# Kernel tuning notes

Measured on AMD Instinct MI355X. Metric: run time of the kernel, lower is better.

Reference implementation:

```python
import jax, jax.numpy as jnp
import numpy as np

B, J, D, H, W, AE, GH, NA, EH, L = 64, 20000, 32, 64, 4, 16, 24, 5000, 128, 32


def _ln(x, g=None, b=None, eps=1e-5):
    mu = x.mean(-1, keepdims=True)
    var = jnp.mean((x - mu) ** 2, axis=-1, keepdims=True)
    y = (x - mu) * jax.lax.rsqrt(var + eps)
    if g is not None:
        y = y * g + b
    return y


def setup_inputs():
    key = jax.random.key(0)
    ks = jax.random.split(key, 12)
    def rn(k, shape, s):
        return (jax.random.normal(k, shape) * s).astype(jnp.float32)
    return {
        "x": jax.random.normal(ks[0], (B, J), jnp.float32),
        "mask": jax.random.randint(ks[1], (B, J), 0, 2, jnp.int32),
        "atse_idx": jax.random.randint(ks[2], (J,), 0, NA, jnp.int32),
        "feature_embedding": jax.random.normal(ks[3], (J, D), jnp.float32),
        "atse_embedding": jax.random.normal(ks[4], (NA, AE), jnp.float32),
        "h_W1": rn(ks[5], (1 + D, H), 0.15), "h_b1": jnp.zeros((H,), jnp.float32),
        "h_ln1_g": jnp.ones((H,), jnp.float32), "h_ln1_b": jnp.zeros((H,), jnp.float32),
        "h_W2": rn(ks[6], (H, D), 0.12), "h_b2": jnp.zeros((D,), jnp.float32),
        "h_ln2_g": jnp.ones((D,), jnp.float32), "h_ln2_b": jnp.zeros((D,), jnp.float32),
        "g_W1": rn(ks[7], (D + AE, GH), 0.14), "g_b1": jnp.zeros((GH,), jnp.float32),
        "g_W2": rn(ks[8], (GH, W), 0.2), "g_b2": jnp.zeros((W,), jnp.float32),
        "c_W": rn(ks[9], (W * D, D), 0.09), "c_b": jnp.zeros((D,), jnp.float32),
        "c_ln_g": jnp.ones((D,), jnp.float32), "c_ln_b": jnp.zeros((D,), jnp.float32),
        "e_W1": rn(ks[10], (D, EH), 0.18), "e_b1": jnp.zeros((EH,), jnp.float32),
        "e_W2": rn(ks[11], (EH, 2 * L), 0.09), "e_b2": jnp.zeros((2 * L,), jnp.float32),
    }


def _forward(x, mask, atse_idx, feature_embedding, atse_embedding,
             h_W1, h_b1, h_ln1_g, h_ln1_b, h_W2, h_b2, h_ln2_g, h_ln2_b,
             g_W1, g_b1, g_W2, g_b2, c_W, c_b, c_ln_g, c_ln_b,
             e_W1, e_b1, e_W2, e_b2):
    TEMP = 1.0  # temperature_fixed=True -> scale = temperature_value
    Bv, Jv = x.shape
    Dv = feature_embedding.shape[1]
    # h-layer on all (b, j) pairs; LayerNorm/ReLU are per-row so this equals the
    # per-sample gather version on observed rows (unobserved rows get zero weight below).
    h_in = jnp.concatenate(
        [x[..., None], jnp.broadcast_to(feature_embedding[None], (Bv, Jv, Dv))], axis=-1)
    h = jax.nn.relu(_ln(h_in @ h_W1 + h_b1, h_ln1_g, h_ln1_b))
    h_out = jax.nn.relu(_ln(h @ h_W2 + h_b2, h_ln2_g, h_ln2_b))  # [B, J, D]
    # gate: [h_out | E_atse(j)] -> W head logits
    ae = atse_embedding[atse_idx]  # [J, AE]
    gate_in = jnp.concatenate(
        [h_out, jnp.broadcast_to(ae[None], (Bv, Jv, ae.shape[1]))], axis=-1)
    raw = jax.nn.relu(gate_in @ g_W1 + g_b1) @ g_W2 + g_b2  # [B, J, W]
    logits = jnp.clip(raw * TEMP, -10.0, 10.0)
    obs = mask.astype(bool)
    masked = jnp.where(obs[..., None], logits, -1e9)
    weights = jax.nn.softmax(masked, axis=1)  # softmax over observed junctions per head
    head_sums = jnp.einsum('bjw,bjd->bwd', weights, h_out)  # [B, W, D]
    Wn, Dn = head_sums.shape[1], head_sums.shape[2]
    combined = jax.nn.relu(_ln(head_sums.reshape(Bv, Wn * Dn) @ c_W + c_b, c_ln_g, c_ln_b))
    combined = jnp.where(obs.any(axis=1)[:, None], combined, 0.0)  # empty-mask rows -> zeros
    # encoder_mlp: scvi FCLayers, 2 layers, LayerNorm (no affine) + ReLU each
    e1 = jax.nn.relu(_ln(combined @ e_W1 + e_b1))
    mu_logvar = jax.nn.relu(_ln(e1 @ e_W2 + e_b2))
    mu, logvar = jnp.split(mu_logvar, 2, axis=-1)
    return mu, logvar


def reference(x, mask, atse_idx, feature_embedding, atse_embedding,
              h_W1, h_b1, h_ln1_g, h_ln1_b, h_W2, h_b2, h_ln2_g, h_ln2_b,
              g_W1, g_b1, g_W2, g_b2, c_W, c_b, c_ln_g, c_ln_b,
              e_W1, e_b1, e_W2, e_b2):
    return _forward(x, mask, atse_idx, feature_embedding, atse_embedding,
                    h_W1, h_b1, h_ln1_g, h_ln1_b, h_W2, h_b2, h_ln2_g, h_ln2_b,
                    g_W1, g_b1, g_W2, g_b2, c_W, c_b, c_ln_g, c_ln_b,
                    e_W1, e_b1, e_W2, e_b2)
```

## Files before the change

kernel.cpp:

```cpp
#include <hip/hip_runtime.h>
#include <hip/hip_bf16.h>
#include <math.h>

#define Bv 64
#define Jv 20000
#define NJT 625
#define NBT 8

typedef __attribute__((ext_vector_type(8))) short short8;
typedef __attribute__((ext_vector_type(4))) float f32x4;

union U8 { short8 s; unsigned int u[4]; };

__device__ __forceinline__ unsigned short f2bf(float f) {
  unsigned int u = __float_as_uint(f);
  u += 0x7FFFu + ((u >> 16) & 1u);
  return (unsigned short)(u >> 16);
}
__device__ __forceinline__ unsigned int pkbf(float a, float b) {
  __hip_bfloat162 h = __float22bfloat162_rn(make_float2(a, b));
  union { __hip_bfloat162 h; unsigned int u; } c;
  c.h = h;
  return c.u;
}
__device__ __forceinline__ float bflo(unsigned int u) { return __uint_as_float(u << 16); }
__device__ __forceinline__ float bfhi(unsigned int u) { return __uint_as_float(u & 0xFFFF0000u); }

__global__ __launch_bounds__(256) void pe_fused(
    const float* __restrict__ x, const int* __restrict__ mask,
    const int* __restrict__ atse_idx, const float* __restrict__ fe,
    const float* __restrict__ ae,
    const float* __restrict__ hW1, const float* __restrict__ hb1,
    const float* __restrict__ hl1g, const float* __restrict__ hl1b,
    const float* __restrict__ hW2, const float* __restrict__ hb2,
    const float* __restrict__ hl2g, const float* __restrict__ hl2b,
    const float* __restrict__ gW1, const float* __restrict__ gb1,
    const float* __restrict__ gW2, const float* __restrict__ gb2,
    float* __restrict__ acc_g, float* __restrict__ se_g) {
  __shared__ __align__(16) float s_pg[32 * 68];
  __shared__ __align__(16) float s_ex[32 * 4];
  __shared__ __align__(16) float s_gb[32 * 28 + 16];
  __shared__ __align__(16) float s_pair[256 * 4];
  __shared__ __align__(16) float s_w0[64], s_w0g[64], s_l1g[64], s_l1b[64];
  __shared__ __align__(16) float s_b2[32], s_l2g[32], s_l2b[32];
  __shared__ __align__(16) float s_gb1[24], s_gW2[96];
  __shared__ float s_gb2[4], s_scal[2];
  __shared__ int s_mk[256];
  __shared__ __align__(16) unsigned short s_gW1bf[32 * 24];
  __shared__ __align__(16) unsigned short s_ovl[256 * 34];

  int tid = threadIdx.x;
  int btile = blockIdx.x;
  int jtile = blockIdx.y;
  int J0 = jtile * 32;
  int lane = tid & 63, wv = tid >> 6;
  int li = lane & 15, quad = lane >> 4;

  float* ovlf = (float*)s_ovl;
  float* s_aeo = ovlf + 2048;
  float* s_gW1bo = ovlf + 2688;
  unsigned short* s_h = s_ovl;

  for (int i = tid; i < 2048; i += 256) ovlf[i] = hW2[i];
  for (int i = tid; i < 768; i += 256) s_gW1bf[i] = f2bf(gW1[i]);
  for (int i = tid; i < 384; i += 256) s_gW1bo[i] = gW1[768 + i];
  if (tid < 96) s_gW2[tid] = gW2[tid];
  if (tid < 64) { s_w0[tid] = hW1[tid]; s_l1g[tid] = hl1g[tid]; s_l1b[tid] = hl1b[tid]; }
  if (tid < 32) { s_b2[tid] = hb2[tid]; s_l2g[tid] = hl2g[tid]; s_l2b[tid] = hl2b[tid]; }
  if (tid < 24) s_gb1[tid] = gb1[tid];
  if (tid < 4) s_gb2[tid] = gb2[tid];
  if (tid < 128) s_gb[(tid >> 2) * 28 + 24 + (tid & 3)] = 0.f;
  if (tid >= 128 && tid < 144) s_gb[32 * 28 + (tid - 128)] = 0.f;
  if (tid < 32) {
    int ai = atse_idx[J0 + tid];
    const float4* av = (const float4*)(ae + (size_t)ai * 16);
#pragma unroll
    for (int q = 0; q < 4; ++q) *(float4*)(s_aeo + tid * 20 + q * 4) = av[q];
  }
  __syncthreads();

  {
    U8 bH;
#pragma unroll
    for (int p = 0; p < 4; ++p) {
      float lo = hW1[(1 + quad * 8 + 2 * p) * 64 + wv * 16 + li];
      float hi = hW1[(1 + quad * 8 + 2 * p + 1) * 64 + wv * 16 + li];
      bH.u[p] = pkbf(lo, hi);
    }
    float hb = hb1[wv * 16 + li];
    f32x4 cP;
#pragma unroll
    for (int mt = 0; mt < 2; ++mt) {
      cP[0] = hb; cP[1] = hb; cP[2] = hb; cP[3] = hb;
      const float* fp = fe + (size_t)(J0 + mt * 16 + li) * 32 + quad * 8;
      float4 f0 = *(const float4*)fp;
      float4 f1 = *(const float4*)(fp + 4);
      U8 aF;
      aF.u[0] = pkbf(f0.x, f0.y); aF.u[1] = pkbf(f0.z, f0.w);
      aF.u[2] = pkbf(f1.x, f1.y); aF.u[3] = pkbf(f1.z, f1.w);
      cP = __builtin_amdgcn_mfma_f32_16x16x32_bf16(aF.s, bH.s, cP, 0, 0, 0);
#pragma unroll
      for (int r = 0; r < 4; ++r)
        s_pg[(mt * 16 + quad * 4 + r) * 68 + wv * 16 + li] = cP[r];
    }
  }
  {
    int jp = tid >> 3, ks = tid & 7;
    int c0 = ks * 3;
    float g3[3] = {s_gb1[c0], s_gb1[c0 + 1], s_gb1[c0 + 2]};
#pragma unroll 4
    for (int a = 0; a < 16; ++a) {
      float Av = s_aeo[jp * 20 + a];
      const float* gr = s_gW1bo + a * 24 + c0;
      g3[0] = fmaf(Av, gr[0], g3[0]);
      g3[1] = fmaf(Av, gr[1], g3[1]);
      g3[2] = fmaf(Av, gr[2], g3[2]);
    }
    s_gb[jp * 28 + c0] = g3[0];
    s_gb[jp * 28 + c0 + 1] = g3[1];
    s_gb[jp * 28 + c0 + 2] = g3[2];
  }
  __syncthreads();

  if (tid < 32) {
    float sp = 0.f, qp = 0.f, dwp = 0.f;
#pragma unroll 8
    for (int k = 0; k < 64; ++k) {
      float p = s_pg[tid * 68 + k];
      float w = s_w0[k];
      sp += p;
      qp = fmaf(p, p, qp);
      dwp = fmaf(p, w, dwp);
    }
    ((float4*)s_ex)[tid] = make_float4(sp, qp, dwp, 0.f);
  } else if (tid == 32) {
    float sw = 0.f, qw = 0.f;
    for (int k = 0; k < 64; ++k) {
      float w = s_w0[k];
      sw += w;
      qw = fmaf(w, w, qw);
    }
    s_scal[0] = sw;
    s_scal[1] = qw;
  } else if (tid >= 64 && tid < 128) {
    s_w0g[tid - 64] = s_w0[tid - 64] * s_l1g[tid - 64];
  }
  __syncthreads();

  {
    int jp = tid >> 3, ks = tid & 7;
    float* pp = s_pg + jp * 68 + ks * 8;
    float4 a0 = *(float4*)pp, a1 = *(float4*)(pp + 4);
    float4 g0 = *(float4*)(s_l1g + ks * 8), g1 = *(float4*)(s_l1g + ks * 8 + 4);
    a0.x *= g0.x; a0.y *= g0.y; a0.z *= g0.z; a0.w *= g0.w;
    a1.x *= g1.x; a1.y *= g1.y; a1.z *= g1.z; a1.w *= g1.w;
    *(float4*)pp = a0;
    *(float4*)(pp + 4) = a1;
  }
  short8 bW2[2][2];
#pragma unroll
  for (int kt = 0; kt < 2; ++kt)
#pragma unroll
    for (int nt = 0; nt < 2; ++nt) {
      U8 t;
#pragma unroll
      for (int p = 0; p < 4; ++p) {
        float lo = ovlf[(kt * 32 + quad * 8 + 2 * p) * 32 + nt * 16 + li];
        float hi = ovlf[(kt * 32 + quad * 8 + 2 * p + 1) * 32 + nt * 16 + li];
        t.u[p] = pkbf(lo, hi);
      }
      bW2[kt][nt] = t.s;
    }
  {
    int j = tid >> 3, b = tid & 7;
    size_t off = (size_t)(btile * 8 + b) * Jv + J0 + j;
    float xv = x[off];
    s_mk[tid] = mask[off];
    float4 ex = ((const float4*)s_ex)[j];
    float mu1 = fmaf(xv, s_scal[0], ex.x) * 0.015625f;
    float Et2 = fmaf(xv * xv, s_scal[1], fmaf(2.0f * xv, ex.z, ex.y)) * 0.015625f;
    float rs1 = rsqrtf(fmaxf(Et2 - mu1 * mu1, 0.f) + 1e-5f);
    *(float4*)(s_pair + tid * 4) = make_float4(xv * rs1, rs1, -mu1 * rs1, 0.f);
  }
  __syncthreads();

  {
    f32x4 cd[4][2];
    float b2a = s_b2[li], b2b = s_b2[16 + li];
#pragma unroll
    for (int t = 0; t < 4; ++t) {
      cd[t][0][0] = b2a; cd[t][0][1] = b2a; cd[t][0][2] = b2a; cd[t][0][3] = b2a;
      cd[t][1][0] = b2b; cd[t][1][1] = b2b; cd[t][1][2] = b2b; cd[t][1][3] = b2b;
    }
#pragma unroll
    for (int kt = 0; kt < 2; ++kt) {
      int base = kt * 32 + quad * 8;
      float4 wg0 = *(const float4*)(s_w0g + base);
      float4 wg1 = *(const float4*)(s_w0g + base + 4);
      float4 gg0 = *(const float4*)(s_l1g + base);
      float4 gg1 = *(const float4*)(s_l1g + base + 4);
      float4 bb0 = *(const float4*)(s_l1b + base);
      float4 bb1 = *(const float4*)(s_l1b + base + 4);
      float wg[8] = {wg0.x, wg0.y, wg0.z, wg0.w, wg1.x, wg1.y, wg1.z, wg1.w};
      float gg[8] = {gg0.x, gg0.y, gg0.z, gg0.w, gg1.x, gg1.y, gg1.z, gg1.w};
      float bb[8] = {bb0.x, bb0.y, bb0.z, bb0.w, bb1.x, bb1.y, bb1.z, bb1.w};
#pragma unroll
      for (int t = 0; t < 4; ++t) {
        int mrow = wv * 64 + t * 16 + li;
        float4 pr = *(const float4*)(s_pair + mrow * 4);
        const float* pgp = s_pg + (mrow >> 3) * 68 + base;
        float4 p0 = *(const float4*)pgp;
        float4 p1 = *(const float4*)(pgp + 4);
        float pv[8] = {p0.x, p0.y, p0.z, p0.w, p1.x, p1.y, p1.z, p1.w};
        float av[8];
#pragma unroll
        for (int i = 0; i < 8; ++i)
          av[i] = fmaxf(fmaf(pr.x, wg[i], fmaf(pr.y, pv[i], fmaf(pr.z, gg[i], bb[i]))), 0.f);
        U8 a8;
        a8.u[0] = pkbf(av[0], av[1]); a8.u[1] = pkbf(av[2], av[3]);
        a8.u[2] = pkbf(av[4], av[5]); a8.u[3] = pkbf(av[6], av[7]);
        cd[t][0] = __builtin_amdgcn_mfma_f32_16x16x32_bf16(a8.s, bW2[kt][0], cd[t][0], 0, 0, 0);
        cd[t][1] = __builtin_amdgcn_mfma_f32_16x16x32_bf16(a8.s, bW2[kt][1], cd[t][1], 0, 0, 0);
      }
    }
    float g0 = s_l2g[li], be0 = s_l2b[li];
    float g1v = s_l2g[16 + li], be1 = s_l2b[16 + li];
#pragma unroll
    for (int t = 0; t < 4; ++t) {
      float sum[4], sq[4];
#pragma unroll
      for (int r = 0; r < 4; ++r) {
        float a = cd[t][0][r], b = cd[t][1][r];
        sum[r] = a + b;
        sq[r] = fmaf(a, a, b * b);
      }
#pragma unroll
      for (int off = 1; off < 16; off <<= 1) {
#pragma unroll
        for (int r = 0; r < 4; ++r) {
          sum[r] += __shfl_xor(sum[r], off);
          sq[r] += __shfl_xor(sq[r], off);
        }
      }
#pragma unroll
      for (int r = 0; r < 4; ++r) {
        float mu = sum[r] * 0.03125f;
        float var = sq[r] * 0.03125f - mu * mu;
        float rs2 = rsqrtf(fmaxf(var, 0.f) + 1e-5f);
        int m = wv * 64 + t * 16 + quad * 4 + r;
        float h0 = fmaxf(fmaf((cd[t][0][r] - mu) * rs2, g0, be0), 0.f);
        float h1 = fmaxf(fmaf((cd[t][1][r] - mu) * rs2, g1v, be1), 0.f);
        s_h[m * 34 + li] = f2bf(h0);
        s_h[m * 34 + 16 + li] = f2bf(h1);
      }
    }
  }

  {
    short8 aG0, aG1;
#pragma unroll
    for (int i = 0; i < 8; ++i) {
      int k = quad * 8 + i;
      aG0[i] = (short)s_gW1bf[k * 24 + li];
      aG1[i] = (li < 8) ? (short)s_gW1bf[k * 24 + 16 + li] : (short)0;
    }
    float4 gw4[2][4];
#pragma unroll
    for (int mt = 0; mt < 2; ++mt)
#pragma unroll
      for (int r = 0; r < 4; ++r) {
        int c = mt * 16 + quad * 4 + r;
        gw4[mt][r] = (c < 24) ? ((const float4*)s_gW2)[c]
                              : make_float4(0.f, 0.f, 0.f, 0.f);
      }
#pragma unroll
    for (int nt = 0; nt < 4; ++nt) {
      int m = wv * 64 + nt * 16 + li;
      U8 bu;
      const unsigned short* hp = s_h + m * 34 + quad * 8;
      bu.u[0] = *(const unsigned int*)(hp + 0);
      bu.u[1] = *(const unsigned int*)(hp + 2);
      bu.u[2] = *(const unsigned int*)(hp + 4);
      bu.u[3] = *(const unsigned int*)(hp + 6);
      int j = m >> 3;
      f32x4 c0, c1;
#pragma unroll
      for (int r = 0; r < 4; ++r) {
        c0[r] = s_gb[j * 28 + quad * 4 + r];
        c1[r] = s_gb[j * 28 + 16 + quad * 4 + r];
      }
      c0 = __builtin_amdgcn_mfma_f32_16x16x32_bf16(aG0, bu.s, c0, 0, 0, 0);
      c1 = __builtin_amdgcn_mfma_f32_16x16x32_bf16(aG1, bu.s, c1, 0, 0, 0);
      float r0 = s_gb2[0], r1 = s_gb2[1], r2 = s_gb2[2], r3 = s_gb2[3];
#pragma unroll
      for (int r = 0; r < 4; ++r) {
        float v0 = fmaxf(c0[r], 0.f);
        float v1 = fmaxf(c1[r], 0.f);
        float4 ga = gw4[0][r], gb = gw4[1][r];
        r0 = fmaf(v0, ga.x, fmaf(v1, gb.x, r0));
        r1 = fmaf(v0, ga.y, fmaf(v1, gb.y, r1));
        r2 = fmaf(v0, ga.z, fmaf(v1, gb.z, r2));
        r3 = fmaf(v0, ga.w, fmaf(v1, gb.w, r3));
      }
      r0 += __shfl_xor(r0, 16); r0 += __shfl_xor(r0, 32);
      r1 += __shfl_xor(r1, 16); r1 += __shfl_xor(r1, 32);
      r2 += __shfl_xor(r2, 16); r2 += __shfl_xor(r2, 32);
      r3 += __shfl_xor(r3, 16); r3 += __shfl_xor(r3, 32);
      r0 = fminf(fmaxf(r0, -10.f), 10.f);
      r1 = fminf(fmaxf(r1, -10.f), 10.f);
      r2 = fminf(fmaxf(r2, -10.f), 10.f);
      r3 = fminf(fmaxf(r3, -10.f), 10.f);
      bool act = (s_mk[m] != 0);
      float e0 = act ? __expf(r0 - 10.f) : 0.f;
      float e1 = act ? __expf(r1 - 10.f) : 0.f;
      float e2 = act ? __expf(r2 - 10.f) : 0.f;
      float e3 = act ? __expf(r3 - 10.f) : 0.f;
      if (quad == 0) *(float4*)(s_pair + m * 4) = make_float4(e0, e1, e2, e3);
    }
  }
  __syncthreads();

  {
    const float* s_e2 = s_pair;
#pragma unroll
    for (int bs = 0; bs < 2; ++bs) {
      int b = wv * 2 + bs;
      float ev[8];
      float separt = 0.f;
#pragma unroll
      for (int i = 0; i < 8; ++i) {
        float v = s_e2[((quad * 8 + i) * 8 + b) * 4 + (li & 3)];
        v = (li < 4) ? v : 0.f;
        ev[i] = v;
        separt += v;
      }
      separt += __shfl_xor(separt, 16);
      separt += __shfl_xor(separt, 32);
      U8 a8;
      a8.u[0] = pkbf(ev[0], ev[1]); a8.u[1] = pkbf(ev[2], ev[3]);
      a8.u[2] = pkbf(ev[4], ev[5]); a8.u[3] = pkbf(ev[6], ev[7]);
#pragma unroll
      for (int half = 0; half < 2; ++half) {
        U8 bh;
#pragma unroll
        for (int p = 0; p < 4; ++p) {
          unsigned int lo = s_h[((quad * 8 + 2 * p) * 8 + b) * 34 + half * 16 + li];
          unsigned int hi = s_h[((quad * 8 + 2 * p + 1) * 8 + b) * 34 + half * 16 + li];
          bh.u[p] = lo | (hi << 16);
        }
        f32x4 c = {0.f, 0.f, 0.f, 0.f};
        c = __builtin_amdgcn_mfma_f32_16x16x32_bf16(a8.s, bh.s, c, 0, 0, 0);
        if (quad == 0) {
          float* dst = acc_g + (size_t)(btile * 8 + b) * 128;
#pragma unroll
          for (int r = 0; r < 4; ++r)
            atomicAdd(dst + r * 32 + half * 16 + li, c[r]);
        }
      }
      if (quad == 0 && li < 4)
        atomicAdd(&se_g[(btile * 8 + b) * 4 + li], separt);
    }
  }
}

__global__ __launch_bounds__(64) void pe_tail(
    const float* __restrict__ acc_g, const float* __restrict__ se_g,
    const float* __restrict__ cW, const float* __restrict__ cb,
    const float* __restrict__ clng, const float* __restrict__ clnb,
    const float* __restrict__ eW1, const float* __restrict__ eb1,
    const float* __restrict__ eW2, const float* __restrict__ eb2,
    float* __restrict__ out) {
  int b = blockIdx.x;
  int lane = threadIdx.x;
  __shared__ float s_hs[128], s_comb[32], s_e1[128];

  float se0 = se_g[b * 4 + 0];
  bool empty = !(se0 > 0.0f);
  float inv[4];
#pragma unroll
  for (int w = 0; w < 4; ++w) {
    float sw = se_g[b * 4 + w];
    inv[w] = empty ? 0.0f : 1.0f / sw;
  }
  s_hs[lane] = acc_g[b * 128 + lane] * inv[lane >> 5];
  s_hs[lane + 64] = acc_g[b * 128 + lane + 64] * inv[(lane + 64) >> 5];
  __syncthreads();

  if (lane < 32) {
    float cp = cb[lane];
#pragma unroll 8
    for (int i = 0; i < 128; ++i) cp = fmaf(s_hs[i], cW[i * 32 + lane], cp);
    float ssum = cp;
#pragma unroll
    for (int off = 16; off > 0; off >>= 1) ssum += __shfl_xor(ssum, off, 32);
    float mu = ssum * (1.0f / 32.0f);
    float dd = cp - mu;
    float sq = dd * dd;
#pragma unroll
    for (int off = 16; off > 0; off >>= 1) sq += __shfl_xor(sq, off, 32);
    float rs = rsqrtf(sq * (1.0f / 32.0f) + 1e-5f);
    float comb = fmaxf(fmaf(dd * rs, clng[lane], clnb[lane]), 0.0f);
    if (empty) comb = 0.0f;
    s_comb[lane] = comb;
  }
  __syncthreads();

  float v0 = eb1[lane], v1 = eb1[lane + 64];
#pragma unroll
  for (int i = 0; i < 32; ++i) {
    float c = s_comb[i];
    v0 = fmaf(c, eW1[i * 128 + lane], v0);
    v1 = fmaf(c, eW1[i * 128 + lane + 64], v1);
  }
  float ssum = v0 + v1;
#pragma unroll
  for (int off = 32; off > 0; off >>= 1) ssum += __shfl_xor(ssum, off, 64);
  float mu = ssum * (1.0f / 128.0f);
  float d0 = v0 - mu, d1 = v1 - mu;
  float sq = fmaf(d0, d0, d1 * d1);
#pragma unroll
  for (int off = 32; off > 0; off >>= 1) sq += __shfl_xor(sq, off, 64);
  float rs = rsqrtf(sq * (1.0f / 128.0f) + 1e-5f);
  s_e1[lane] = fmaxf(d0 * rs, 0.0f);
  s_e1[lane + 64] = fmaxf(d1 * rs, 0.0f);
  __syncthreads();

  float v = eb2[lane];
#pragma unroll 8
  for (int i = 0; i < 128; ++i) v = fmaf(s_e1[i], eW2[i * 64 + lane], v);
  ssum = v;
#pragma unroll
  for (int off = 32; off > 0; off >>= 1) ssum += __shfl_xor(ssum, off, 64);
  mu = ssum * (1.0f / 64.0f);
  float dv = v - mu;
  sq = dv * dv;
#pragma unroll
  for (int off = 32; off > 0; off >>= 1) sq += __shfl_xor(sq, off, 64);
  rs = rsqrtf(sq * (1.0f / 64.0f) + 1e-5f);
  float o = fmaxf(dv * rs, 0.0f);
  if (lane < 32)
    out[b * 32 + lane] = o;
  else
    out[Bv * 32 + b * 32 + (lane - 32)] = o;
}

extern "C" void kernel_launch(void* const* d_in, const int* in_sizes, int n_in,
                              void* d_out, int out_size, void* d_ws, size_t ws_size,
                              hipStream_t stream) {
  const float* x    = (const float*)d_in[0];
  const int* mask   = (const int*)d_in[1];
  const int* atse   = (const int*)d_in[2];
  const float* fe   = (const float*)d_in[3];
  const float* ae   = (const float*)d_in[4];
  const float* hW1  = (const float*)d_in[5];
  const float* hb1  = (const float*)d_in[6];
  const float* hl1g = (const float*)d_in[7];
  const float* hl1b = (const float*)d_in[8];
  const float* hW2  = (const float*)d_in[9];
  const float* hb2  = (const float*)d_in[10];
  const float* hl2g = (const float*)d_in[11];
  const float* hl2b = (const float*)d_in[12];
  const float* gW1  = (const float*)d_in[13];
  const float* gb1  = (const float*)d_in[14];
  const float* gW2  = (const float*)d_in[15];
  const float* gb2  = (const float*)d_in[16];
  const float* cW   = (const float*)d_in[17];
  const float* cb   = (const float*)d_in[18];
  const float* clng = (const float*)d_in[19];
  const float* clnb = (const float*)d_in[20];
  const float* eW1  = (const float*)d_in[21];
  const float* eb1  = (const float*)d_in[22];
  const float* eW2  = (const float*)d_in[23];
  const float* eb2  = (const float*)d_in[24];
  float* out = (float*)d_out;

  float* ws = (float*)d_ws;
  float* accg = ws;
  float* seg  = accg + Bv * 128;

  hipMemsetAsync(accg, 0, (Bv * 128 + Bv * 4) * sizeof(float), stream);

  pe_fused<<<dim3(NBT, NJT), dim3(256), 0, stream>>>(
      x, mask, atse, fe, ae, hW1, hb1, hl1g, hl1b, hW2, hb2, hl2g, hl2b,
      gW1, gb1, gW2, gb2, accg, seg);
  pe_tail<<<dim3(Bv), dim3(64), 0, stream>>>(
      accg, seg, cW, cb, clng, clnb, eW1, eb1, eW2, eb2, out);
}
```

Before: 232.2 us.

## Make fused kernel persistent over five J-tiles with register-held accumulators

```diff
diff --git a/kernel.cpp b/kernel.cpp
--- a/kernel.cpp
+++ b/kernel.cpp
@@ -4,8 +4,9 @@
 
 #define Bv 64
 #define Jv 20000
-#define NJT 625
 #define NBT 8
+#define NYB 125
+#define ITERS 5
 
 typedef __attribute__((ext_vector_type(8))) short short8;
 typedef __attribute__((ext_vector_type(4))) float f32x4;
@@ -23,8 +24,6 @@
   c.h = h;
   return c.u;
 }
-__device__ __forceinline__ float bflo(unsigned int u) { return __uint_as_float(u << 16); }
-__device__ __forceinline__ float bfhi(unsigned int u) { return __uint_as_float(u & 0xFFFF0000u); }
 
 __global__ __launch_bounds__(256) void pe_fused(
     const float* __restrict__ x, const int* __restrict__ mask,
@@ -39,29 +38,26 @@
     float* __restrict__ acc_g, float* __restrict__ se_g) {
   __shared__ __align__(16) float s_pg[32 * 68];
   __shared__ __align__(16) float s_ex[32 * 4];
-  __shared__ __align__(16) float s_gb[32 * 28 + 16];
+  __shared__ __align__(16) float s_gb[32 * 24 + 16];
   __shared__ __align__(16) float s_pair[256 * 4];
   __shared__ __align__(16) float s_w0[64], s_w0g[64], s_l1g[64], s_l1b[64];
   __shared__ __align__(16) float s_b2[32], s_l2g[32], s_l2b[32];
   __shared__ __align__(16) float s_gb1[24], s_gW2[96];
   __shared__ float s_gb2[4], s_scal[2];
-  __shared__ int s_mk[256];
+  __shared__ __align__(16) float s_gW1bo[384];
+  __shared__ unsigned char s_mk[256];
   __shared__ __align__(16) unsigned short s_gW1bf[32 * 24];
   __shared__ __align__(16) unsigned short s_ovl[256 * 34];
 
   int tid = threadIdx.x;
   int btile = blockIdx.x;
-  int jtile = blockIdx.y;
-  int J0 = jtile * 32;
+  int ytile = blockIdx.y;
   int lane = tid & 63, wv = tid >> 6;
   int li = lane & 15, quad = lane >> 4;
-
-  float* ovlf = (float*)s_ovl;
-  float* s_aeo = ovlf + 2048;
-  float* s_gW1bo = ovlf + 2688;
   unsigned short* s_h = s_ovl;
 
-  for (int i = tid; i < 2048; i += 256) ovlf[i] = hW2[i];
+#define AEROW(j) ((float*)((char*)s_ovl + ((j) >> 3) * 4352 + 3712) + ((j) & 7) * 20)
+
   for (int i = tid; i < 768; i += 256) s_gW1bf[i] = f2bf(gW1[i]);
   for (int i = tid; i < 384; i += 256) s_gW1bo[i] = gW1[768 + i];
   if (tid < 96) s_gW2[tid] = gW2[tid];
@@ -69,94 +65,8 @@
   if (tid < 32) { s_b2[tid] = hb2[tid]; s_l2g[tid] = hl2g[tid]; s_l2b[tid] = hl2b[tid]; }
   if (tid < 24) s_gb1[tid] = gb1[tid];
   if (tid < 4) s_gb2[tid] = gb2[tid];
-  if (tid < 128) s_gb[(tid >> 2) * 28 + 24 + (tid & 3)] = 0.f;
-  if (tid >= 128 && tid < 144) s_gb[32 * 28 + (tid - 128)] = 0.f;
-  if (tid < 32) {
-    int ai = atse_idx[J0 + tid];
-    const float4* av = (const float4*)(ae + (size_t)ai * 16);
-#pragma unroll
-    for (int q = 0; q < 4; ++q) *(float4*)(s_aeo + tid * 20 + q * 4) = av[q];
-  }
-  __syncthreads();
-
-  {
-    U8 bH;
-#pragma unroll
-    for (int p = 0; p < 4; ++p) {
-      float lo = hW1[(1 + quad * 8 + 2 * p) * 64 + wv * 16 + li];
-      float hi = hW1[(1 + quad * 8 + 2 * p + 1) * 64 + wv * 16 + li];
-      bH.u[p] = pkbf(lo, hi);
-    }
-    float hb = hb1[wv * 16 + li];
-    f32x4 cP;
-#pragma unroll
-    for (int mt = 0; mt < 2; ++mt) {
-      cP[0] = hb; cP[1] = hb; cP[2] = hb; cP[3] = hb;
-      const float* fp = fe + (size_t)(J0 + mt * 16 + li) * 32 + quad * 8;
-      float4 f0 = *(const float4*)fp;
-      float4 f1 = *(const float4*)(fp + 4);
-      U8 aF;
-      aF.u[0] = pkbf(f0.x, f0.y); aF.u[1] = pkbf(f0.z, f0.w);
-      aF.u[2] = pkbf(f1.x, f1.y); aF.u[3] = pkbf(f1.z, f1.w);
-      cP = __builtin_amdgcn_mfma_f32_16x16x32_bf16(aF.s, bH.s, cP, 0, 0, 0);
-#pragma unroll
-      for (int r = 0; r < 4; ++r)
-        s_pg[(mt * 16 + quad * 4 + r) * 68 + wv * 16 + li] = cP[r];
-    }
-  }
-  {
-    int jp = tid >> 3, ks = tid & 7;
-    int c0 = ks * 3;
-    float g3[3] = {s_gb1[c0], s_gb1[c0 + 1], s_gb1[c0 + 2]};
-#pragma unroll 4
-    for (int a = 0; a < 16; ++a) {
-      float Av = s_aeo[jp * 20 + a];
-      const float* gr = s_gW1bo + a * 24 + c0;
-      g3[0] = fmaf(Av, gr[0], g3[0]);
-      g3[1] = fmaf(Av, gr[1], g3[1]);
-      g3[2] = fmaf(Av, gr[2], g3[2]);
-    }
-    s_gb[jp * 28 + c0] = g3[0];
-    s_gb[jp * 28 + c0 + 1] = g3[1];
-    s_gb[jp * 28 + c0 + 2] = g3[2];
-  }
-  __syncthreads();
-
-  if (tid < 32) {
-    float sp = 0.f, qp = 0.f, dwp = 0.f;
-#pragma unroll 8
-    for (int k = 0; k < 64; ++k) {
-      float p = s_pg[tid * 68 + k];
-      float w = s_w0[k];
-      sp += p;
-      qp = fmaf(p, p, qp);
-      dwp = fmaf(p, w, dwp);
-    }
-    ((float4*)s_ex)[tid] = make_float4(sp, qp, dwp, 0.f);
-  } else if (tid == 32) {
-    float sw = 0.f, qw = 0.f;
-    for (int k = 0; k < 64; ++k) {
-      float w = s_w0[k];
-      sw += w;
-      qw = fmaf(w, w, qw);
-    }
-    s_scal[0] = sw;
-    s_scal[1] = qw;
-  } else if (tid >= 64 && tid < 128) {
-    s_w0g[tid - 64] = s_w0[tid - 64] * s_l1g[tid - 64];
-  }
-  __syncthreads();
-
-  {
-    int jp = tid >> 3, ks = tid & 7;
-    float* pp = s_pg + jp * 68 + ks * 8;
-    float4 a0 = *(float4*)pp, a1 = *(float4*)(pp + 4);
-    float4 g0 = *(float4*)(s_l1g + ks * 8), g1 = *(float4*)(s_l1g + ks * 8 + 4);
-    a0.x *= g0.x; a0.y *= g0.y; a0.z *= g0.z; a0.w *= g0.w;
-    a1.x *= g1.x; a1.y *= g1.y; a1.z *= g1.z; a1.w *= g1.w;
-    *(float4*)pp = a0;
-    *(float4*)(pp + 4) = a1;
-  }
+  if (tid >= 224 && tid < 240) s_gb[32 * 24 + (tid - 224)] = 0.f;
+
   short8 bW2[2][2];
 #pragma unroll
   for (int kt = 0; kt < 2; ++kt)
@@ -165,202 +75,301 @@
       U8 t;
 #pragma unroll
       for (int p = 0; p < 4; ++p) {
-        float lo = ovlf[(kt * 32 + quad * 8 + 2 * p) * 32 + nt * 16 + li];
-        float hi = ovlf[(kt * 32 + quad * 8 + 2 * p + 1) * 32 + nt * 16 + li];
+        float lo = hW2[(kt * 32 + quad * 8 + 2 * p) * 32 + nt * 16 + li];
+        float hi = hW2[(kt * 32 + quad * 8 + 2 * p + 1) * 32 + nt * 16 + li];
         t.u[p] = pkbf(lo, hi);
       }
       bW2[kt][nt] = t.s;
     }
-  {
-    int j = tid >> 3, b = tid & 7;
-    size_t off = (size_t)(btile * 8 + b) * Jv + J0 + j;
-    float xv = x[off];
-    s_mk[tid] = mask[off];
-    float4 ex = ((const float4*)s_ex)[j];
-    float mu1 = fmaf(xv, s_scal[0], ex.x) * 0.015625f;
-    float Et2 = fmaf(xv * xv, s_scal[1], fmaf(2.0f * xv, ex.z, ex.y)) * 0.015625f;
-    float rs1 = rsqrtf(fmaxf(Et2 - mu1 * mu1, 0.f) + 1e-5f);
-    *(float4*)(s_pair + tid * 4) = make_float4(xv * rs1, rs1, -mu1 * rs1, 0.f);
-  }
+  U8 bH;
+#pragma unroll
+  for (int p = 0; p < 4; ++p) {
+    float lo = hW1[(1 + quad * 8 + 2 * p) * 64 + wv * 16 + li];
+    float hi = hW1[(1 + quad * 8 + 2 * p + 1) * 64 + wv * 16 + li];
+    bH.u[p] = pkbf(lo, hi);
+  }
+  float hb = hb1[wv * 16 + li];
+
   __syncthreads();
-
-  {
-    f32x4 cd[4][2];
-    float b2a = s_b2[li], b2b = s_b2[16 + li];
-#pragma unroll
-    for (int t = 0; t < 4; ++t) {
-      cd[t][0][0] = b2a; cd[t][0][1] = b2a; cd[t][0][2] = b2a; cd[t][0][3] = b2a;
-      cd[t][1][0] = b2b; cd[t][1][1] = b2b; cd[t][1][2] = b2b; cd[t][1][3] = b2b;
-    }
-#pragma unroll
-    for (int kt = 0; kt < 2; ++kt) {
-      int base = kt * 32 + quad * 8;
-      float4 wg0 = *(const float4*)(s_w0g + base);
-      float4 wg1 = *(const float4*)(s_w0g + base + 4);
-      float4 gg0 = *(const float4*)(s_l1g + base);
-      float4 gg1 = *(const float4*)(s_l1g + base + 4);
-      float4 bb0 = *(const float4*)(s_l1b + base);
-      float4 bb1 = *(const float4*)(s_l1b + base + 4);
-      float wg[8] = {wg0.x, wg0.y, wg0.z, wg0.w, wg1.x, wg1.y, wg1.z, wg1.w};
-      float gg[8] = {gg0.x, gg0.y, gg0.z, gg0.w, gg1.x, gg1.y, gg1.z, gg1.w};
-      float bb[8] = {bb0.x, bb0.y, bb0.z, bb0.w, bb1.x, bb1.y, bb1.z, bb1.w};
+  if (tid < 64) s_w0g[tid] = s_w0[tid] * s_l1g[tid];
+  if (tid == 64) {
+    float sw = 0.f, qw = 0.f;
+    for (int k = 0; k < 64; ++k) { float w = s_w0[k]; sw += w; qw = fmaf(w, w, qw); }
+    s_scal[0] = sw; s_scal[1] = qw;
+  }
+
+  f32x4 racc[2][2];
+#pragma unroll
+  for (int a = 0; a < 2; ++a)
+#pragma unroll
+    for (int c = 0; c < 2; ++c) {
+      racc[a][c][0] = 0.f; racc[a][c][1] = 0.f; racc[a][c][2] = 0.f; racc[a][c][3] = 0.f;
+    }
+  float seacc[2] = {0.f, 0.f};
+
+  int jp8 = tid >> 3, b8 = tid & 7;
+
+  for (int it = 0; it < ITERS; ++it) {
+    int J0 = (ytile * ITERS + it) * 32;
+
+    if (tid < 32) {
+      int ai = atse_idx[J0 + tid];
+      const float4* av4 = (const float4*)(ae + (size_t)ai * 16);
+      float* ar = AEROW(tid);
+#pragma unroll
+      for (int q = 0; q < 4; ++q) *(float4*)(ar + q * 4) = av4[q];
+    }
+    size_t xoff = (size_t)(btile * 8 + b8) * Jv + J0 + jp8;
+    float xv = x[xoff];
+    int mk = mask[xoff];
+    {
+      f32x4 cP;
+#pragma unroll
+      for (int mt = 0; mt < 2; ++mt) {
+        cP[0] = hb; cP[1] = hb; cP[2] = hb; cP[3] = hb;
+        const float* fp = fe + (size_t)(J0 + mt * 16 + li) * 32 + quad * 8;
+        float4 f0 = *(const float4*)fp;
+        float4 f1 = *(const float4*)(fp + 4);
+        U8 aF;
+        aF.u[0] = pkbf(f0.x, f0.y); aF.u[1] = pkbf(f0.z, f0.w);
+        aF.u[2] = pkbf(f1.x, f1.y); aF.u[3] = pkbf(f1.z, f1.w);
+        cP = __builtin_amdgcn_mfma_f32_16x16x32_bf16(aF.s, bH.s, cP, 0, 0, 0);
+#pragma unroll
+        for (int r = 0; r < 4; ++r)
+          s_pg[(mt * 16 + quad * 4 + r) * 68 + wv * 16 + li] = cP[r];
+      }
+    }
+    __syncthreads();
+
+    {
+      int c0 = b8 * 3;
+      float g3[3] = {s_gb1[c0], s_gb1[c0 + 1], s_gb1[c0 + 2]};
+      const float* ar = AEROW(jp8);
+#pragma unroll 4
+      for (int a = 0; a < 16; ++a) {
+        float Av = ar[a];
+        const float* gr = s_gW1bo + a * 24 + c0;
+        g3[0] = fmaf(Av, gr[0], g3[0]);
+        g3[1] = fmaf(Av, gr[1], g3[1]);
+        g3[2] = fmaf(Av, gr[2], g3[2]);
+      }
+      s_gb[jp8 * 24 + c0] = g3[0];
+      s_gb[jp8 * 24 + c0 + 1] = g3[1];
+      s_gb[jp8 * 24 + c0 + 2] = g3[2];
+    }
+    {
+      const float* pp = s_pg + jp8 * 68 + b8 * 8;
+      float4 p0 = *(const float4*)pp, p1 = *(const float4*)(pp + 4);
+      float4 wa = *(const float4*)(s_w0 + b8 * 8), wb = *(const float4*)(s_w0 + b8 * 8 + 4);
+      float sp = p0.x + p0.y + p0.z + p0.w + p1.x + p1.y + p1.z + p1.w;
+      float qp = fmaf(p0.x, p0.x, fmaf(p0.y, p0.y, fmaf(p0.z, p0.z, p0.w * p0.w)));
+      qp = fmaf(p1.x, p1.x, fmaf(p1.y, p1.y, fmaf(p1.z, p1.z, fmaf(p1.w, p1.w, qp))));
+      float dwp = fmaf(p0.x, wa.x, fmaf(p0.y, wa.y, fmaf(p0.z, wa.z, p0.w * wa.w)));
+      dwp = fmaf(p1.x, wb.x, fmaf(p1.y, wb.y, fmaf(p1.z, wb.z, fmaf(p1.w, wb.w, dwp))));
+#pragma unroll
+      for (int off = 1; off < 8; off <<= 1) {
+        sp += __shfl_xor(sp, off);
+        qp += __shfl_xor(qp, off);
+        dwp += __shfl_xor(dwp, off);
+      }
+      if (b8 == 0) ((float4*)s_ex)[jp8] = make_float4(sp, qp, dwp, 0.f);
+    }
+    {
+      float4 exv = ((const float4*)s_ex)[jp8];
+      float mu1 = fmaf(xv, s_scal[0], exv.x) * 0.015625f;
+      float Et2 = fmaf(xv * xv, s_scal[1], fmaf(2.0f * xv, exv.z, exv.y)) * 0.015625f;
+      float rs1 = rsqrtf(fmaxf(Et2 - mu1 * mu1, 0.f) + 1e-5f);
+      *(float4*)(s_pair + tid * 4) = make_float4(xv * rs1, rs1, -mu1 * rs1, 0.f);
+      s_mk[tid] = (unsigned char)mk;
+    }
+
+    {
+      f32x4 cd[4][2];
+      float b2a = s_b2[li], b2b = s_b2[16 + li];
 #pragma unroll
       for (int t = 0; t < 4; ++t) {
-        int mrow = wv * 64 + t * 16 + li;
-        float4 pr = *(const float4*)(s_pair + mrow * 4);
-        const float* pgp = s_pg + (mrow >> 3) * 68 + base;
-        float4 p0 = *(const float4*)pgp;
-        float4 p1 = *(const float4*)(pgp + 4);
-        float pv[8] = {p0.x, p0.y, p0.z, p0.w, p1.x, p1.y, p1.z, p1.w};
-        float av[8];
-#pragma unroll
-        for (int i = 0; i < 8; ++i)
-          av[i] = fmaxf(fmaf(pr.x, wg[i], fmaf(pr.y, pv[i], fmaf(pr.z, gg[i], bb[i]))), 0.f);
+        cd[t][0][0] = b2a; cd[t][0][1] = b2a; cd[t][0][2] = b2a; cd[t][0][3] = b2a;
+        cd[t][1][0] = b2b; cd[t][1][1] = b2b; cd[t][1][2] = b2b; cd[t][1][3] = b2b;
+      }
+#pragma unroll
+      for (int kt = 0; kt < 2; ++kt) {
+        int base = kt * 32 + quad * 8;
+        float4 wg0 = *(const float4*)(s_w0g + base);
+        float4 wg1 = *(const float4*)(s_w0g + base + 4);
+        float4 gg0 = *(const float4*)(s_l1g + base);
+        float4 gg1 = *(const float4*)(s_l1g + base + 4);
+        float4 bb0 = *(const float4*)(s_l1b + base);
+        float4 bb1 = *(const float4*)(s_l1b + base + 4);
+        float wg[8] = {wg0.x, wg0.y, wg0.z, wg0.w, wg1.x, wg1.y, wg1.z, wg1.w};
+        float gg[8] = {gg0.x, gg0.y, gg0.z, gg0.w, gg1.x, gg1.y, gg1.z, gg1.w};
+        float bb[8] = {bb0.x, bb0.y, bb0.z, bb0.w, bb1.x, bb1.y, bb1.z, bb1.w};
+#pragma unroll
+        for (int t = 0; t < 4; ++t) {
+          int mrow = wv * 64 + t * 16 + li;
+          float4 pr = *(const float4*)(s_pair + mrow * 4);
+          const float* pgp = s_pg + (mrow >> 3) * 68 + base;
+          float4 p0 = *(const float4*)pgp;
+          float4 p1 = *(const float4*)(pgp + 4);
+          float pv[8] = {p0.x, p0.y, p0.z, p0.w, p1.x, p1.y, p1.z, p1.w};
+          float av[8];
+#pragma unroll
+          for (int i = 0; i < 8; ++i)
+            av[i] = fmaxf(fmaf(fmaf(pr.y, pv[i], pr.z), gg[i], fmaf(pr.x, wg[i], bb[i])), 0.f);
+          U8 a8;
+          a8.u[0] = pkbf(av[0], av[1]); a8.u[1] = pkbf(av[2], av[3]);
+          a8.u[2] = pkbf(av[4], av[5]); a8.u[3] = pkbf(av[6], av[7]);
+          cd[t][0] = __builtin_amdgcn_mfma_f32_16x16x32_bf16(a8.s, bW2[kt][0], cd[t][0], 0, 0, 0);
+          cd[t][1] = __builtin_amdgcn_mfma_f32_16x16x32_bf16(a8.s, bW2[kt][1], cd[t][1], 0, 0, 0);
+        }
+      }
+      float g0 = s_l2g[li], be0 = s_l2b[li];
+      float g1v = s_l2g[16 + li], be1 = s_l2b[16 + li];
+#pragma unroll
+      for (int t = 0; t < 4; ++t) {
+        float sum[4], sq[4];
+#pragma unroll
+        for (int r = 0; r < 4; ++r) {
+          float a = cd[t][0][r], b = cd[t][1][r];
+          sum[r] = a + b;
+          sq[r] = fmaf(a, a, b * b);
+        }
+#pragma unroll
+        for (int off = 1; off < 16; off <<= 1) {
+#pragma unroll
+          for (int r = 0; r < 4; ++r) {
+            sum[r] += __shfl_xor(sum[r], off);
+            sq[r] += __shfl_xor(sq[r], off);
+          }
+        }
+#pragma unroll
+        for (int r = 0; r < 4; ++r) {
+          float mu = sum[r] * 0.03125f;
+          float var = sq[r] * 0.03125f - mu * mu;
+          float rs2 = rsqrtf(fmaxf(var, 0.f) + 1e-5f);
+          int m = wv * 64 + t * 16 + quad * 4 + r;
+          float h0 = fmaxf(fmaf((cd[t][0][r] - mu) * rs2, g0, be0), 0.f);
+          float h1 = fmaxf(fmaf((cd[t][1][r] - mu) * rs2, g1v, be1), 0.f);
+          s_h[m * 34 + li] = f2bf(h0);
+          s_h[m * 34 + 16 + li] = f2bf(h1);
+        }
+      }
+    }
+
+    {
+      short8 aG0, aG1;
+#pragma unroll
+      for (int i = 0; i < 8; ++i) {
+        int k = quad * 8 + i;
+        aG0[i] = (short)s_gW1bf[k * 24 + li];
+        aG1[i] = (li < 8) ? (short)s_gW1bf[k * 24 + 16 + li] : (short)0;
+      }
+      float4 gw4[2][4];
+#pragma unroll
+      for (int mt = 0; mt < 2; ++mt)
+#pragma unroll
+        for (int r = 0; r < 4; ++r) {
+          int c = mt * 16 + quad * 4 + r;
+          gw4[mt][r] = (c < 24) ? ((const float4*)s_gW2)[c]
+                                : make_float4(0.f, 0.f, 0.f, 0.f);
+        }
+#pragma unroll
+      for (int nt = 0; nt < 4; ++nt) {
+        int m = wv * 64 + nt * 16 + li;
+        U8 bu;
+        const unsigned short* hp = s_h + m * 34 + quad * 8;
+        bu.u[0] = *(const unsigned int*)(hp + 0);
+        bu.u[1] = *(const unsigned int*)(hp + 2);
+        bu.u[2] = *(const unsigned int*)(hp + 4);
+        bu.u[3] = *(const unsigned int*)(hp + 6);
+        int j = m >> 3;
+        f32x4 c0, c1;
+#pragma unroll
+        for (int r = 0; r < 4; ++r) {
+          c0[r] = s_gb[j * 24 + quad * 4 + r];
+          c1[r] = s_gb[j * 24 + 16 + quad * 4 + r];
+        }
+        c0 = __builtin_amdgcn_mfma_f32_16x16x32_bf16(aG0, bu.s, c0, 0, 0, 0);
+        c1 = __builtin_amdgcn_mfma_f32_16x16x32_bf16(aG1, bu.s, c1, 0, 0, 0);
+        float r0 = s_gb2[0], r1 = s_gb2[1], r2 = s_gb2[2], r3 = s_gb2[3];
+#pragma unroll
+        for (int r = 0; r < 4; ++r) {
+          float v0 = fmaxf(c0[r], 0.f);
+          float v1 = fmaxf(c1[r], 0.f);
+          float4 ga = gw4[0][r], gb = gw4[1][r];
+          r0 = fmaf(v0, ga.x, fmaf(v1, gb.x, r0));
+          r1 = fmaf(v0, ga.y, fmaf(v1, gb.y, r1));
+          r2 = fmaf(v0, ga.z, fmaf(v1, gb.z, r2));
+          r3 = fmaf(v0, ga.w, fmaf(v1, gb.w, r3));
+        }
+        r0 += __shfl_xor(r0, 16); r0 += __shfl_xor(r0, 32);
+        r1 += __shfl_xor(r1, 16); r1 += __shfl_xor(r1, 32);
+        r2 += __shfl_xor(r2, 16); r2 += __shfl_xor(r2, 32);
+        r3 += __shfl_xor(r3, 16); r3 += __shfl_xor(r3, 32);
+        r0 = fminf(fmaxf(r0, -10.f), 10.f);
+        r1 = fminf(fmaxf(r1, -10.f), 10.f);
+        r2 = fminf(fmaxf(r2, -10.f), 10.f);
+        r3 = fminf(fmaxf(r3, -10.f), 10.f);
+        bool act = (s_mk[m] != 0);
+        float e0 = act ? __expf(r0 - 10.f) : 0.f;
+        float e1 = act ? __expf(r1 - 10.f) : 0.f;
+        float e2 = act ? __expf(r2 - 10.f) : 0.f;
+        float e3 = act ? __expf(r3 - 10.f) : 0.f;
+        if (quad == 0) *(float4*)(s_pair + m * 4) = make_float4(e0, e1, e2, e3);
+      }
+    }
+    __syncthreads();
+
+    {
+      const float* s_e2 = s_pair;
+#pragma unroll
+      for (int bs = 0; bs < 2; ++bs) {
+        int b = wv * 2 + bs;
+        float ev[8];
+        float sep = 0.f;
+#pragma unroll
+        for (int i = 0; i < 8; ++i) {
+          float v = s_e2[((quad * 8 + i) * 8 + b) * 4 + (li & 3)];
+          v = (li < 4) ? v : 0.f;
+          ev[i] = v;
+          sep += v;
+        }
+        seacc[bs] += sep;
         U8 a8;
-        a8.u[0] = pkbf(av[0], av[1]); a8.u[1] = pkbf(av[2], av[3]);
-        a8.u[2] = pkbf(av[4], av[5]); a8.u[3] = pkbf(av[6], av[7]);
-        cd[t][0] = __builtin_amdgcn_mfma_f32_16x16x32_bf16(a8.s, bW2[kt][0], cd[t][0], 0, 0, 0);
-        cd[t][1] = __builtin_amdgcn_mfma_f32_16x16x32_bf16(a8.s, bW2[kt][1], cd[t][1], 0, 0, 0);
-      }
-    }
-    float g0 = s_l2g[li], be0 = s_l2b[li];
-    float g1v = s_l2g[16 + li], be1 = s_l2b[16 + li];
-#pragma unroll
-    for (int t = 0; t < 4; ++t) {
-      float sum[4], sq[4];
-#pragma unroll
-      for (int r = 0; r < 4; ++r) {
-        float a = cd[t][0][r], b = cd[t][1][r];
-        sum[r] = a + b;
-        sq[r] = fmaf(a, a, b * b);
-      }
-#pragma unroll
-      for (int off = 1; off < 16; off <<= 1) {
-#pragma unroll
-        for (int r = 0; r < 4; ++r) {
-          sum[r] += __shfl_xor(sum[r], off);
-          sq[r] += __shfl_xor(sq[r], off);
-        }
-      }
-#pragma unroll
-      for (int r = 0; r < 4; ++r) {
-        float mu = sum[r] * 0.03125f;
-        float var = sq[r] * 0.03125f - mu * mu;
-        float rs2 = rsqrtf(fmaxf(var, 0.f) + 1e-5f);
-        int m = wv * 64 + t * 16 + quad * 4 + r;
-        float h0 = fmaxf(fmaf((cd[t][0][r] - mu) * rs2, g0, be0), 0.f);
-        float h1 = fmaxf(fmaf((cd[t][1][r] - mu) * rs2, g1v, be1), 0.f);
-        s_h[m * 34 + li] = f2bf(h0);
-        s_h[m * 34 + 16 + li] = f2bf(h1);
-      }
-    }
-  }
-
-  {
-    short8 aG0, aG1;
-#pragma unroll
-    for (int i = 0; i < 8; ++i) {
-      int k = quad * 8 + i;
-      aG0[i] = (short)s_gW1bf[k * 24 + li];
-      aG1[i] = (li < 8) ? (short)s_gW1bf[k * 24 + 16 + li] : (short)0;
-    }
-    float4 gw4[2][4];
-#pragma unroll
-    for (int mt = 0; mt < 2; ++mt)
-#pragma unroll
-      for (int r = 0; r < 4; ++r) {
-        int c = mt * 16 + quad * 4 + r;
-        gw4[mt][r] = (c < 24) ? ((const float4*)s_gW2)[c]
-                              : make_float4(0.f, 0.f, 0.f, 0.f);
-      }
-#pragma unroll
-    for (int nt = 0; nt < 4; ++nt) {
-      int m = wv * 64 + nt * 16 + li;
-      U8 bu;
-      const unsigned short* hp = s_h + m * 34 + quad * 8;
-      bu.u[0] = *(const unsigned int*)(hp + 0);
-      bu.u[1] = *(const unsigned int*)(hp + 2);
-      bu.u[2] = *(const unsigned int*)(hp + 4);
-      bu.u[3] = *(const unsigned int*)(hp + 6);
-      int j = m >> 3;
-      f32x4 c0, c1;
-#pragma unroll
-      for (int r = 0; r < 4; ++r) {
-        c0[r] = s_gb[j * 28 + quad * 4 + r];
-        c1[r] = s_gb[j * 28 + 16 + quad * 4 + r];
-      }
-      c0 = __builtin_amdgcn_mfma_f32_16x16x32_bf16(aG0, bu.s, c0, 0, 0, 0);
-      c1 = __builtin_amdgcn_mfma_f32_16x16x32_bf16(aG1, bu.s, c1, 0, 0, 0);
-      float r0 = s_gb2[0], r1 = s_gb2[1], r2 = s_gb2[2], r3 = s_gb2[3];
-#pragma unroll
-      for (int r = 0; r < 4; ++r) {
-        float v0 = fmaxf(c0[r], 0.f);
-        float v1 = fmaxf(c1[r], 0.f);
-        float4 ga = gw4[0][r], gb = gw4[1][r];
-        r0 = fmaf(v0, ga.x, fmaf(v1, gb.x, r0));
-        r1 = fmaf(v0, ga.y, fmaf(v1, gb.y, r1));
-        r2 = fmaf(v0, ga.z, fmaf(v1, gb.z, r2));
-        r3 = fmaf(v0, ga.w, fmaf(v1, gb.w, r3));
-      }
-      r0 += __shfl_xor(r0, 16); r0 += __shfl_xor(r0, 32);
-      r1 += __shfl_xor(r1, 16); r1 += __shfl_xor(r1, 32);
-      r2 += __shfl_xor(r2, 16); r2 += __shfl_xor(r2, 32);
-      r3 += __shfl_xor(r3, 16); r3 += __shfl_xor(r3, 32);
-      r0 = fminf(fmaxf(r0, -10.f), 10.f);
-      r1 = fminf(fmaxf(r1, -10.f), 10.f);
-      r2 = fminf(fmaxf(r2, -10.f), 10.f);
-      r3 = fminf(fmaxf(r3, -10.f), 10.f);
-      bool act = (s_mk[m] != 0);
-      float e0 = act ? __expf(r0 - 10.f) : 0.f;
-      float e1 = act ? __expf(r1 - 10.f) : 0.f;
-      float e2 = act ? __expf(r2 - 10.f) : 0.f;
-      float e3 = act ? __expf(r3 - 10.f) : 0.f;
-      if (quad == 0) *(float4*)(s_pair + m * 4) = make_float4(e0, e1, e2, e3);
-    }
-  }
-  __syncthreads();
-
-  {
-    const float* s_e2 = s_pair;
-#pragma unroll
-    for (int bs = 0; bs < 2; ++bs) {
-      int b = wv * 2 + bs;
-      float ev[8];
-      float separt = 0.f;
-#pragma unroll
-      for (int i = 0; i < 8; ++i) {
-        float v = s_e2[((quad * 8 + i) * 8 + b) * 4 + (li & 3)];
-        v = (li < 4) ? v : 0.f;
-        ev[i] = v;
-        separt += v;
-      }
-      separt += __shfl_xor(separt, 16);
-      separt += __shfl_xor(separt, 32);
-      U8 a8;
-      a8.u[0] = pkbf(ev[0], ev[1]); a8.u[1] = pkbf(ev[2], ev[3]);
-      a8.u[2] = pkbf(ev[4], ev[5]); a8.u[3] = pkbf(ev[6], ev[7]);
-#pragma unroll
-      for (int half = 0; half < 2; ++half) {
-        U8 bh;
-#pragma unroll
-        for (int p = 0; p < 4; ++p) {
-          unsigned int lo = s_h[((quad * 8 + 2 * p) * 8 + b) * 34 + half * 16 + li];
-          unsigned int hi = s_h[((quad * 8 + 2 * p + 1) * 8 + b) * 34 + half * 16 + li];
-          bh.u[p] = lo | (hi << 16);
-        }
-        f32x4 c = {0.f, 0.f, 0.f, 0.f};
-        c = __builtin_amdgcn_mfma_f32_16x16x32_bf16(a8.s, bh.s, c, 0, 0, 0);
-        if (quad == 0) {
-          float* dst = acc_g + (size_t)(btile * 8 + b) * 128;
-#pragma unroll
-          for (int r = 0; r < 4; ++r)
-            atomicAdd(dst + r * 32 + half * 16 + li, c[r]);
-        }
-      }
-      if (quad == 0 && li < 4)
-        atomicAdd(&se_g[(btile * 8 + b) * 4 + li], separt);
-    }
-  }
+        a8.u[0] = pkbf(ev[0], ev[1]); a8.u[1] = pkbf(ev[2], ev[3]);
+        a8.u[2] = pkbf(ev[4], ev[5]); a8.u[3] = pkbf(ev[6], ev[7]);
+#pragma unroll
+        for (int half = 0; half < 2; ++half) {
+          U8 bh;
+#pragma unroll
+          for (int p = 0; p < 4; ++p) {
+            unsigned int lo = s_h[((quad * 8 + 2 * p) * 8 + b) * 34 + half * 16 + li];
+            unsigned int hi = s_h[((quad * 8 + 2 * p + 1) * 8 + b) * 34 + half * 16 + li];
+            bh.u[p] = lo | (hi << 16);
+          }
+          racc[bs][half] = __builtin_amdgcn_mfma_f32_16x16x32_bf16(a8.s, bh.s, racc[bs][half], 0, 0, 0);
+        }
+      }
+    }
+    __syncthreads();
+  }
+
+#pragma unroll
+  for (int bs = 0; bs < 2; ++bs) {
+    float se = seacc[bs];
+    se += __shfl_xor(se, 16);
+    se += __shfl_xor(se, 32);
+    if (quad == 0) {
+      int bg = btile * 8 + wv * 2 + bs;
+      float* dst = acc_g + (size_t)bg * 128;
+#pragma unroll
+      for (int half = 0; half < 2; ++half)
+#pragma unroll
+        for (int r = 0; r < 4; ++r)
+          atomicAdd(dst + r * 32 + half * 16 + li, racc[bs][half][r]);
+      if (li < 4) atomicAdd(&se_g[bg * 4 + li], se);
+    }
+  }
+#undef AEROW
 }
 
 __global__ __launch_bounds__(64) void pe_tail(
@@ -480,7 +489,7 @@
 
   hipMemsetAsync(accg, 0, (Bv * 128 + Bv * 4) * sizeof(float), stream);
 
-  pe_fused<<<dim3(NBT, NJT), dim3(256), 0, stream>>>(
+  pe_fused<<<dim3(NBT, NYB), dim3(256), 0, stream>>>(
       x, mask, atse, fe, ae, hW1, hb1, hl1g, hl1b, hW2, hb2, hl2g, hl2b,
       gW1, gb1, gW2, gb2, accg, seg);
   pe_tail<<<dim3(Bv), dim3(64), 0, stream>>>(
```

New measurement: 226.7 us. 1.02x faster.
